# Optimization experiments

Measured on AMD Instinct MI355X. Metric: run time of the kernel, lower is better.

## Reference

```python
import jax, jax.numpy as jnp
import numpy as np

EPS = 1e-5

def _proj_bn(x, w, b, gamma, beta, mean, var):
    # 1x1 conv: [B,C,H,W] x [O,C] -> [B,O,H,W], then inference BatchNorm
    y = jnp.einsum('bchw,oc->bohw', x, w) + b[None, :, None, None]
    inv = gamma / jnp.sqrt(var + EPS)
    return y * inv[None, :, None, None] + (beta - mean * inv)[None, :, None, None]


def setup_inputs() -> dict:
    key = jax.random.key(0)
    ks = jax.random.split(key, 20)
    B, C, H, W = 4, 256, 64, 64
    Cq = C // 8
    s = lambda k, shp, sc: jax.random.normal(k, shp, dtype=jnp.float32) * sc
    inp = {
        'x1': s(ks[0], (B, C, H, W), 1.0),
        'x2': s(ks[1], (B, C, H, W), 1.0),
        'q_w': s(ks[2], (Cq, C), 0.05), 'q_b': s(ks[3], (Cq,), 0.02),
        'q_gamma': 1.0 + s(ks[4], (Cq,), 0.02), 'q_beta': s(ks[5], (Cq,), 0.02),
        'q_mean': s(ks[6], (Cq,), 0.1), 'q_var': jnp.abs(1.0 + s(ks[7], (Cq,), 0.1)),
        'k_w': s(ks[8], (Cq, C), 0.05), 'k_b': s(ks[9], (Cq,), 0.02),
        'k_gamma': 1.0 + s(ks[10], (Cq,), 0.02), 'k_beta': s(ks[11], (Cq,), 0.02),
        'k_mean': s(ks[12], (Cq,), 0.1), 'k_var': jnp.abs(1.0 + s(ks[13], (Cq,), 0.1)),
        'v_w': s(ks[14], (C, C), 0.05), 'v_b': s(ks[15], (C,), 0.02),
        'v_gamma': 1.0 + s(ks[16], (C,), 0.02), 'v_beta': s(ks[17], (C,), 0.02),
        'v_mean': s(ks[18], (C,), 0.1), 'v_var': jnp.abs(1.0 + s(ks[19], (C,), 0.1)),
    }
    return inp


def reference(x1, x2, q_w, q_b, q_gamma, q_beta, q_mean, q_var,
              k_w, k_b, k_gamma, k_beta, k_mean, k_var,
              v_w, v_b, v_gamma, v_beta, v_mean, v_var):
    B, C, H, W = x1.shape
    N = H * W
    dqk = C // 8
    q = _proj_bn(x1, q_w, q_b, q_gamma, q_beta, q_mean, q_var).reshape(B, dqk, N)  # [B,dqk,N]
    k = _proj_bn(x2, k_w, k_b, k_gamma, k_beta, k_mean, k_var).reshape(B, dqk, N)  # [B,dqk,N]
    v = _proj_bn(x2, v_w, v_b, v_gamma, v_beta, v_mean, v_var).reshape(B, C, N)    # [B,C,N]
    scale = 1.0 / np.sqrt(dqk).astype(np.float32)
    energy = jnp.einsum('bdm,bdn->bmn', q, k) * scale        # [B,N,N]
    attn = jax.nn.softmax(energy, axis=-1)
    out = jnp.einsum('bcn,bmn->bcm', v, attn)                # [B,C,N]
    return out.reshape(B, C, H, W)
```

## Files before the change

kernel.cpp:

```cpp
#include <hip/hip_runtime.h>

using short8   = __attribute__((ext_vector_type(8))) short;
using f32x4    = __attribute__((ext_vector_type(4))) float;
using ushort4v = __attribute__((ext_vector_type(4))) unsigned short;

#define BN_EPS 1e-5f
#define ATT_SCALE_LOG2E 0.2550348347988049f

__device__ __forceinline__ unsigned short f2bf(float f) {
    union { float f; unsigned u; } v; v.f = f;
    return (unsigned short)((v.u + 0x7FFFu + ((v.u >> 16) & 1u)) >> 16);
}

__device__ __forceinline__ unsigned pack2bf(float a, float b) {
    union { float f; unsigned u; } ua, ub; ua.f = a; ub.f = b;
    return __builtin_amdgcn_perm(ub.u + 0x8000u, ua.u + 0x8000u, 0x07060302u);
}

__device__ __forceinline__ void glds16(const void* gp, void* lp) {
    __builtin_amdgcn_global_load_lds(
        (const __attribute__((address_space(1))) unsigned*)gp,
        (__attribute__((address_space(3))) unsigned*)lp, 16, 0, 0);
}

__global__ void prep_kernel(
    const float* __restrict__ qw, const float* __restrict__ qb,
    const float* __restrict__ qg, const float* __restrict__ qbe,
    const float* __restrict__ qm, const float* __restrict__ qv,
    const float* __restrict__ kw, const float* __restrict__ kb,
    const float* __restrict__ kg, const float* __restrict__ kbe,
    const float* __restrict__ km, const float* __restrict__ kvv,
    const float* __restrict__ vw, const float* __restrict__ vb,
    const float* __restrict__ vg, const float* __restrict__ vbe,
    const float* __restrict__ vm, const float* __restrict__ vv,
    unsigned short* __restrict__ wq, float* __restrict__ scale,
    float* __restrict__ off)
{
    int r = blockIdx.x;
    int t = threadIdx.x;
    const float *wsrc, *g, *be, *mn, *vr, *bi;
    int rl;
    if (r < 32)      { rl = r;      wsrc = qw; g = qg; be = qbe; mn = qm; vr = qv;  bi = qb; }
    else if (r < 64) { rl = r - 32; wsrc = kw; g = kg; be = kbe; mn = km; vr = kvv; bi = kb; }
    else             { rl = r - 64; wsrc = vw; g = vg; be = vbe; mn = vm; vr = vv;  bi = vb; }

    float4 w4 = *(const float4*)(wsrc + rl * 256 + t * 4);
    ushort4v o;
    o.x = f2bf(w4.x); o.y = f2bf(w4.y); o.z = f2bf(w4.z); o.w = f2bf(w4.w);
    *(ushort4v*)(wq + r * 256 + t * 4) = o;

    if (t == 0) {
        float inv = g[rl] * rsqrtf(vr[rl] + BN_EPS);
        float ofv = bi[rl] * inv + be[rl] - mn[rl] * inv;
        float s = (r < 32) ? ATT_SCALE_LOG2E : 1.0f;
        scale[r] = inv * s;
        off[r]   = ofv * s;
    }
}

#define XT_PITCH 264

__global__ __launch_bounds__(256, 4) void proj_kernel(
    const float* __restrict__ x1, const float* __restrict__ x2,
    const unsigned short* __restrict__ wq,
    const float* __restrict__ scale, const float* __restrict__ off,
    unsigned short* __restrict__ q_t, unsigned short* __restrict__ k_t,
    unsigned short* __restrict__ v_ws)
{
    __shared__ __align__(16) unsigned short Xt[64 * XT_PITCH];
    int bx = blockIdx.x;
    int g  = bx >> 8;
    int t2 = bx & 255;
    int nt = t2 & 63;
    int b  = t2 >> 6;
    int n0 = nt * 64;
    int tid = threadIdx.x;
    int wv = tid >> 6, lane = tid & 63;
    int m16 = lane & 15, qd = lane >> 4;

    const float* xb = ((g == 0) ? x1 : x2) + (size_t)b * 256 * 4096 + n0 + lane;

    #pragma unroll 2
    for (int i = 0; i < 8; ++i) {
        int o = wv * 8 + i;
        const float* src = xb + (size_t)(o * 8) * 4096;
        uint4 dw;
        dw.x = pack2bf(src[0],                src[(size_t)1 * 4096]);
        dw.y = pack2bf(src[(size_t)2 * 4096], src[(size_t)3 * 4096]);
        dw.z = pack2bf(src[(size_t)4 * 4096], src[(size_t)5 * 4096]);
        dw.w = pack2bf(src[(size_t)6 * 4096], src[(size_t)7 * 4096]);
        *(uint4*)&Xt[lane * XT_PITCH + o * 8] = dw;
    }
    __syncthreads();

    f32x4 zero4 = {0.f, 0.f, 0.f, 0.f};

    if (g < 2) {
        int rb = g * 32;
        f32x4 acc0 = zero4, acc1 = zero4;
        #pragma unroll 2
        for (int s = 0; s < 8; ++s) {
            short8 w0 = *(const short8*)(wq + (size_t)(rb +      m16) * 256 + s * 32 + qd * 8);
            short8 w1 = *(const short8*)(wq + (size_t)(rb + 16 + m16) * 256 + s * 32 + qd * 8);
            short8 xf = *(const short8*)&Xt[(16 * wv + m16) * XT_PITCH + s * 32 + qd * 8];
            acc0 = __builtin_amdgcn_mfma_f32_16x16x32_bf16(w0, xf, acc0, 0, 0, 0);
            acc1 = __builtin_amdgcn_mfma_f32_16x16x32_bf16(w1, xf, acc1, 0, 0, 0);
        }
        unsigned short* dst = (g == 0) ? q_t : k_t;
        int ncol = n0 + 16 * wv + m16;
        #pragma unroll
        for (int tm = 0; tm < 2; ++tm) {
            f32x4 acc = tm ? acc1 : acc0;
            int r0 = 16 * tm + 4 * qd;
            float4 sc = *(const float4*)(scale + rb + r0);
            float4 of = *(const float4*)(off   + rb + r0);
            ushort4v o;
            o.x = f2bf(acc.x * sc.x + of.x);
            o.y = f2bf(acc.y * sc.y + of.y);
            o.z = f2bf(acc.z * sc.z + of.z);
            o.w = f2bf(acc.w * sc.w + of.w);
            *(ushort4v*)(dst + ((size_t)b * 4096 + ncol) * 32 + r0) = o;
        }
    } else {
        f32x4 acc[4][4];
        #pragma unroll
        for (int rr = 0; rr < 4; ++rr)
            #pragma unroll
            for (int tm = 0; tm < 4; ++tm) acc[rr][tm] = zero4;
        #pragma unroll 1
        for (int s = 0; s < 8; ++s) {
            short8 xf[4];
            #pragma unroll
            for (int tm = 0; tm < 4; ++tm)
                xf[tm] = *(const short8*)&Xt[(16 * tm + m16) * XT_PITCH + s * 32 + qd * 8];
            #pragma unroll
            for (int rr = 0; rr < 4; ++rr) {
                short8 wf = *(const short8*)(wq + (size_t)(64 + rr * 64 + 16 * wv + m16) * 256 + s * 32 + qd * 8);
                #pragma unroll
                for (int tm = 0; tm < 4; ++tm)
                    acc[rr][tm] = __builtin_amdgcn_mfma_f32_16x16x32_bf16(xf[tm], wf, acc[rr][tm], 0, 0, 0);
            }
        }
        unsigned short* vt = v_ws + ((size_t)b * 32 + (nt >> 1)) * 32768;
        int h = nt & 1;
        #pragma unroll
        for (int rr = 0; rr < 4; ++rr) {
            int c = rr * 64 + 16 * wv + m16;
            float sc = scale[64 + c], of = off[64 + c];
            #pragma unroll
            for (int tm = 0; tm < 4; ++tm) {
                int gg = 4 * tm + qd;
                int gs = (gg & 8) | ((gg & 7) ^ (c & 7));
                ushort4v o;
                o.x = f2bf(acc[rr][tm].x * sc + of);
                o.y = f2bf(acc[rr][tm].y * sc + of);
                o.z = f2bf(acc[rr][tm].z * sc + of);
                o.w = f2bf(acc[rr][tm].w * sc + of);
                *(ushort4v*)(vt + c * 128 + gs * 8 + h * 4) = o;
            }
        }
    }
}

__global__ __launch_bounds__(256, 2) void flash_kernel(
    const unsigned short* __restrict__ q_t, const unsigned short* __restrict__ k_t,
    const unsigned short* __restrict__ v_ws, float* __restrict__ out)
{
    __shared__ __align__(16) unsigned char Vb[2][32768];
    __shared__ __align__(16) float Lsh[256];

    int bx = blockIdx.x;
    int cg = (bx >> 2) & 1;
    int b  = bx & 3;
    int qg = bx >> 3;
    int q0 = qg * 64;
    int cb = cg * 128;

    int tid = threadIdx.x;
    int wv  = tid >> 6, lane = tid & 63;
    int m16 = lane & 15, qd = lane >> 4;

    const char* vpb = (const char*)v_ws + (size_t)b * 2097152 + (size_t)cb * 256;
    int vgo[8], vl[8];
    #pragma unroll
    for (int u = 0; u < 8; ++u) {
        int i = (wv * 8 + u) * 64 + lane;
        vgo[u] = i * 16;
        vl[u]  = (wv * 8 + u) * 1024;
    }
    int gw = wv * 4 + qd;
    int gs = (gw & 8) | ((gw & 7) ^ (m16 & 7));
    int vro[8];
    #pragma unroll
    for (int ct = 0; ct < 8; ++ct) vro[ct] = (ct * 16 + m16) * 256 + gs * 16;

    const unsigned short* kbase = k_t + ((size_t)b * 4096 + wv * 16 + m16) * 32 + qd * 8;

    const unsigned short* qb = q_t + ((size_t)b * 4096 + q0) * 32;
    short8 Qf[4];
    #pragma unroll
    for (int qt = 0; qt < 4; ++qt)
        Qf[qt] = *(const short8*)(qb + (size_t)(qt * 16 + m16) * 32 + qd * 8);

    f32x4 zero4 = {0.f, 0.f, 0.f, 0.f};
    f32x4 acc[4][8];
    #pragma unroll
    for (int qt = 0; qt < 4; ++qt)
        #pragma unroll
        for (int ct = 0; ct < 8; ++ct) acc[qt][ct] = zero4;
    float lsum[4] = {0.f, 0.f, 0.f, 0.f};

    #pragma unroll
    for (int u = 0; u < 8; ++u) glds16(vpb + vgo[u], (char*)Vb + vl[u]);
    short8 KA0 = *(const short8*)kbase;
    short8 KA1 = *(const short8*)(kbase + 2048);
    short8 KB0 = KA0, KB1 = KA1;

    auto body = [&](const short8& K0c, const short8& K1c,
                    short8& K0n, short8& K1n,
                    char* Vcur, char* Vnxt, int ep) {
        asm volatile("s_waitcnt vmcnt(0)\n\ts_barrier" ::: "memory");

        if (ep < 31) {
            const char* vs = vpb + (size_t)(ep + 1) * 65536;
            #pragma unroll
            for (int u = 0; u < 8; ++u) glds16(vs + vgo[u], Vnxt + vl[u]);
            const unsigned short* ks = kbase + (size_t)(ep + 1) * 4096;
            K0n = *(const short8*)ks;
            K1n = *(const short8*)(ks + 2048);
        }

        f32x4 SA[4], SB[4];
        #pragma unroll
        for (int qt = 0; qt < 4; ++qt) {
            SA[qt] = __builtin_amdgcn_mfma_f32_16x16x32_bf16(K0c, Qf[qt], zero4, 0, 0, 0);
            SB[qt] = __builtin_amdgcn_mfma_f32_16x16x32_bf16(K1c, Qf[qt], zero4, 0, 0, 0);
        }

        short8 ap[4];
        #pragma unroll
        for (int qt = 0; qt < 4; ++qt) {
            float a0 = __builtin_amdgcn_exp2f(SA[qt].x), a1 = __builtin_amdgcn_exp2f(SA[qt].y);
            float a2 = __builtin_amdgcn_exp2f(SA[qt].z), a3 = __builtin_amdgcn_exp2f(SA[qt].w);
            float b0 = __builtin_amdgcn_exp2f(SB[qt].x), b1 = __builtin_amdgcn_exp2f(SB[qt].y);
            float b2 = __builtin_amdgcn_exp2f(SB[qt].z), b3 = __builtin_amdgcn_exp2f(SB[qt].w);
            lsum[qt] += ((a0 + a1) + (a2 + a3)) + ((b0 + b1) + (b2 + b3));
            union { uint4 u; short8 s; } w;
            w.u.x = pack2bf(a0, a1); w.u.y = pack2bf(a2, a3);
            w.u.z = pack2bf(b0, b1); w.u.w = pack2bf(b2, b3);
            ap[qt] = w.s;
        }

        __builtin_amdgcn_s_setprio(1);
        #pragma unroll
        for (int ct = 0; ct < 8; ++ct) {
            short8 Vf = *(const short8*)(Vcur + vro[ct]);
            #pragma unroll
            for (int qt = 0; qt < 4; ++qt)
                acc[qt][ct] = __builtin_amdgcn_mfma_f32_16x16x32_bf16(ap[qt], Vf, acc[qt][ct], 0, 0, 0);
        }
        __builtin_amdgcn_s_setprio(0);
    };

    #pragma unroll 1
    for (int ep = 0; ep < 32; ep += 2) {
        body(KA0, KA1, KB0, KB1, (char*)Vb[0], (char*)Vb[1], ep);
        body(KB0, KB1, KA0, KA1, (char*)Vb[1], (char*)Vb[0], ep + 1);
    }

    #pragma unroll
    for (int qt = 0; qt < 4; ++qt) {
        float l = lsum[qt];
        l += __shfl_xor(l, 16);
        l += __shfl_xor(l, 32);
        if (lane < 16) Lsh[wv * 64 + qt * 16 + lane] = l;
    }

    char* X = (char*)Vb;
    asm volatile("s_waitcnt vmcnt(0) lgkmcnt(0)\n\ts_barrier" ::: "memory");
    if (wv >= 2) {
        char* dst = X + (size_t)(wv - 2) * 32768;
        #pragma unroll
        for (int qt = 0; qt < 4; ++qt)
            #pragma unroll
            for (int ct = 0; ct < 8; ++ct)
                *(f32x4*)(dst + (qt * 8 + ct) * 1024 + lane * 16) = acc[qt][ct];
    }
    asm volatile("s_waitcnt lgkmcnt(0)\n\ts_barrier" ::: "memory");
    if (wv < 2) {
        const char* src = X + (size_t)wv * 32768;
        #pragma unroll
        for (int qt = 0; qt < 4; ++qt)
            #pragma unroll
            for (int ct = 0; ct < 8; ++ct)
                acc[qt][ct] += *(const f32x4*)(src + (qt * 8 + ct) * 1024 + lane * 16);
    }
    asm volatile("s_waitcnt lgkmcnt(0)\n\ts_barrier" ::: "memory");
    if (wv == 1) {
        char* dst = X + 32768;
        #pragma unroll
        for (int qt = 0; qt < 4; ++qt)
            #pragma unroll
            for (int ct = 0; ct < 8; ++ct)
                *(f32x4*)(dst + (qt * 8 + ct) * 1024 + lane * 16) = acc[qt][ct];
    }
    asm volatile("s_waitcnt lgkmcnt(0)\n\ts_barrier" ::: "memory");
    if (wv == 0) {
        const char* src = X + 32768;
        #pragma unroll
        for (int qt = 0; qt < 4; ++qt)
            #pragma unroll
            for (int ct = 0; ct < 8; ++ct)
                acc[qt][ct] += *(const f32x4*)(src + (qt * 8 + ct) * 1024 + lane * 16);

        #pragma unroll
        for (int qt = 0; qt < 4; ++qt) {
            f32x4 s4 = *(const f32x4*)&Lsh[qt * 16 + qd * 4];
            s4 += *(const f32x4*)&Lsh[64  + qt * 16 + qd * 4];
            s4 += *(const f32x4*)&Lsh[128 + qt * 16 + qd * 4];
            s4 += *(const f32x4*)&Lsh[192 + qt * 16 + qd * 4];
            f32x4 inv4;
            inv4.x = __builtin_amdgcn_rcpf(s4.x);
            inv4.y = __builtin_amdgcn_rcpf(s4.y);
            inv4.z = __builtin_amdgcn_rcpf(s4.z);
            inv4.w = __builtin_amdgcn_rcpf(s4.w);
            #pragma unroll
            for (int ct = 0; ct < 8; ++ct) {
                float* ob = out + ((size_t)(b * 256 + cb + ct * 16 + m16)) * 4096
                                + q0 + qt * 16 + qd * 4;
                float4 o;
                o.x = acc[qt][ct].x * inv4.x;
                o.y = acc[qt][ct].y * inv4.y;
                o.z = acc[qt][ct].z * inv4.z;
                o.w = acc[qt][ct].w * inv4.w;
                *(float4*)ob = o;
            }
        }
    }
}

extern "C" void kernel_launch(void* const* d_in, const int* in_sizes, int n_in,
                              void* d_out, int out_size, void* d_ws, size_t ws_size,
                              hipStream_t stream)
{
    const float* x1  = (const float*)d_in[0];
    const float* x2  = (const float*)d_in[1];
    const float* qw  = (const float*)d_in[2];
    const float* qb  = (const float*)d_in[3];
    const float* qg  = (const float*)d_in[4];
    const float* qbe = (const float*)d_in[5];
    const float* qm  = (const float*)d_in[6];
    const float* qv  = (const float*)d_in[7];
    const float* kw  = (const float*)d_in[8];
    const float* kb  = (const float*)d_in[9];
    const float* kg  = (const float*)d_in[10];
    const float* kbe = (const float*)d_in[11];
    const float* km  = (const float*)d_in[12];
    const float* kvv = (const float*)d_in[13];
    const float* vw  = (const float*)d_in[14];
    const float* vb  = (const float*)d_in[15];
    const float* vg  = (const float*)d_in[16];
    const float* vbe = (const float*)d_in[17];
    const float* vm  = (const float*)d_in[18];
    const float* vv  = (const float*)d_in[19];

    char* ws = (char*)d_ws;
    unsigned short* wq   = (unsigned short*)(ws + 0);
    float*          scale= (float*)(ws + 163840);
    float*          off  = (float*)(ws + 165120);
    unsigned short* q_t  = (unsigned short*)(ws + 166400);
    unsigned short* k_t  = (unsigned short*)(ws + 166400 + 1048576);
    unsigned short* v_ws = (unsigned short*)(ws + 166400 + 2097152);

    prep_kernel<<<320, 64, 0, stream>>>(qw, qb, qg, qbe, qm, qv,
                                        kw, kb, kg, kbe, km, kvv,
                                        vw, vb, vg, vbe, vm, vv,
                                        wq, scale, off);
    proj_kernel<<<768, 256, 0, stream>>>(x1, x2, wq, scale, off, q_t, k_t, v_ws);
    flash_kernel<<<512, 256, 0, stream>>>(q_t, k_t, v_ws, (float*)d_out);
}
```

Before: 173.2 us.

## Software-pipeline attention loop: compute next tile's QK/exp during current PV

Restructures the main attention loop so the QK^T MFMA and exp2 for tile ep+1 are computed in the same iteration as the PV MFMAs for tile ep, with a prologue and epilogue. K and V loads are prefetched two tiles ahead, using partial vmcnt waits. All V fragments are read from LDS up front, and a second barrier guards reuse of the V buffer. This aims to hide exp/softmax latency and global-load latency behind matrix work, at the cost of more registers (two P fragment sets, eight V fragments) and an extra barrier per step.

```diff
diff --git a/kernel.cpp b/kernel.cpp
--- a/kernel.cpp
+++ b/kernel.cpp
@@ -210,62 +210,111 @@
         for (int ct = 0; ct < 8; ++ct) acc[qt][ct] = zero4;
     float lsum[4] = {0.f, 0.f, 0.f, 0.f};
 
-    #pragma unroll
-    for (int u = 0; u < 8; ++u) glds16(vpb + vgo[u], (char*)Vb + vl[u]);
     short8 KA0 = *(const short8*)kbase;
     short8 KA1 = *(const short8*)(kbase + 2048);
-    short8 KB0 = KA0, KB1 = KA1;
-
-    auto body = [&](const short8& K0c, const short8& K1c,
-                    short8& K0n, short8& K1n,
-                    char* Vcur, char* Vnxt, int ep) {
-        asm volatile("s_waitcnt vmcnt(0)\n\ts_barrier" ::: "memory");
-
-        if (ep < 31) {
-            const char* vs = vpb + (size_t)(ep + 1) * 65536;
-            #pragma unroll
-            for (int u = 0; u < 8; ++u) glds16(vs + vgo[u], Vnxt + vl[u]);
-            const unsigned short* ks = kbase + (size_t)(ep + 1) * 4096;
-            K0n = *(const short8*)ks;
-            K1n = *(const short8*)(ks + 2048);
-        }
+    short8 KB0 = *(const short8*)(kbase + 4096);
+    short8 KB1 = *(const short8*)(kbase + 4096 + 2048);
+    #pragma unroll
+    for (int u = 0; u < 8; ++u) glds16(vpb + vgo[u], (char*)Vb + vl[u]);
+    #pragma unroll
+    for (int u = 0; u < 8; ++u) glds16(vpb + 65536 + vgo[u], (char*)Vb[1] + vl[u]);
+    asm volatile("s_waitcnt vmcnt(16)" ::: "memory");
+
+    short8 apA[4], apB[4];
+    #pragma unroll
+    for (int qt = 0; qt < 4; ++qt) {
+        f32x4 SA = __builtin_amdgcn_mfma_f32_16x16x32_bf16(KA0, Qf[qt], zero4, 0, 0, 0);
+        f32x4 SB = __builtin_amdgcn_mfma_f32_16x16x32_bf16(KA1, Qf[qt], zero4, 0, 0, 0);
+        float a0 = __builtin_amdgcn_exp2f(SA.x), a1 = __builtin_amdgcn_exp2f(SA.y);
+        float a2 = __builtin_amdgcn_exp2f(SA.z), a3 = __builtin_amdgcn_exp2f(SA.w);
+        float b0 = __builtin_amdgcn_exp2f(SB.x), b1 = __builtin_amdgcn_exp2f(SB.y);
+        float b2 = __builtin_amdgcn_exp2f(SB.z), b3 = __builtin_amdgcn_exp2f(SB.w);
+        lsum[qt] += ((a0 + a1) + (a2 + a3)) + ((b0 + b1) + (b2 + b3));
+        union { uint4 u; short8 s; } w;
+        w.u.x = pack2bf(a0, a1); w.u.y = pack2bf(a2, a3);
+        w.u.z = pack2bf(b0, b1); w.u.w = pack2bf(b2, b3);
+        apA[qt] = w.s;
+    }
+
+    auto body = [&](short8 (&apC)[4], short8 (&apN)[4],
+                    const short8& Ku0, const short8& Ku1,
+                    short8& Kl0, short8& Kl1, int ep) {
+        asm volatile("s_waitcnt vmcnt(8)\n\ts_barrier" ::: "memory");
+        char* Vcur = (char*)Vb + (size_t)(ep & 1) * 32768;
+
+        short8 Vf[8];
+        #pragma unroll
+        for (int ct = 0; ct < 8; ++ct)
+            Vf[ct] = *(const short8*)(Vcur + vro[ct]);
 
         f32x4 SA[4], SB[4];
-        #pragma unroll
-        for (int qt = 0; qt < 4; ++qt) {
-            SA[qt] = __builtin_amdgcn_mfma_f32_16x16x32_bf16(K0c, Qf[qt], zero4, 0, 0, 0);
-            SB[qt] = __builtin_amdgcn_mfma_f32_16x16x32_bf16(K1c, Qf[qt], zero4, 0, 0, 0);
-        }
-
-        short8 ap[4];
-        #pragma unroll
-        for (int qt = 0; qt < 4; ++qt) {
-            float a0 = __builtin_amdgcn_exp2f(SA[qt].x), a1 = __builtin_amdgcn_exp2f(SA[qt].y);
-            float a2 = __builtin_amdgcn_exp2f(SA[qt].z), a3 = __builtin_amdgcn_exp2f(SA[qt].w);
-            float b0 = __builtin_amdgcn_exp2f(SB[qt].x), b1 = __builtin_amdgcn_exp2f(SB[qt].y);
-            float b2 = __builtin_amdgcn_exp2f(SB[qt].z), b3 = __builtin_amdgcn_exp2f(SB[qt].w);
-            lsum[qt] += ((a0 + a1) + (a2 + a3)) + ((b0 + b1) + (b2 + b3));
-            union { uint4 u; short8 s; } w;
-            w.u.x = pack2bf(a0, a1); w.u.y = pack2bf(a2, a3);
-            w.u.z = pack2bf(b0, b1); w.u.w = pack2bf(b2, b3);
-            ap[qt] = w.s;
+        bool doQK = (ep < 31);
+        if (doQK) {
+            #pragma unroll
+            for (int qt = 0; qt < 4; ++qt) {
+                SA[qt] = __builtin_amdgcn_mfma_f32_16x16x32_bf16(Ku0, Qf[qt], zero4, 0, 0, 0);
+                SB[qt] = __builtin_amdgcn_mfma_f32_16x16x32_bf16(Ku1, Qf[qt], zero4, 0, 0, 0);
+            }
+        }
+
+        asm volatile("s_waitcnt lgkmcnt(0)\n\ts_barrier" ::: "memory");
+
+        if (ep < 30) {
+            const unsigned short* ks = kbase + (size_t)(ep + 2) * 4096;
+            Kl0 = *(const short8*)ks;
+            Kl1 = *(const short8*)(ks + 2048);
+            const char* vs = vpb + (size_t)(ep + 2) * 65536;
+            #pragma unroll
+            for (int u = 0; u < 8; ++u) glds16(vs + vgo[u], Vcur + vl[u]);
+        }
+
+        if (doQK) {
+            #pragma unroll
+            for (int qt = 0; qt < 4; ++qt) {
+                float a0 = __builtin_amdgcn_exp2f(SA[qt].x), a1 = __builtin_amdgcn_exp2f(SA[qt].y);
+                float a2 = __builtin_amdgcn_exp2f(SA[qt].z), a3 = __builtin_amdgcn_exp2f(SA[qt].w);
+                float b0 = __builtin_amdgcn_exp2f(SB[qt].x), b1 = __builtin_amdgcn_exp2f(SB[qt].y);
+                float b2 = __builtin_amdgcn_exp2f(SB[qt].z), b3 = __builtin_amdgcn_exp2f(SB[qt].w);
+                lsum[qt] += ((a0 + a1) + (a2 + a3)) + ((b0 + b1) + (b2 + b3));
+                union { uint4 u; short8 s; } w;
+                w.u.x = pack2bf(a0, a1); w.u.y = pack2bf(a2, a3);
+                w.u.z = pack2bf(b0, b1); w.u.w = pack2bf(b2, b3);
+                apN[qt] = w.s;
+            }
         }
 
         __builtin_amdgcn_s_setprio(1);
         #pragma unroll
         for (int ct = 0; ct < 8; ++ct) {
-            short8 Vf = *(const short8*)(Vcur + vro[ct]);
             #pragma unroll
             for (int qt = 0; qt < 4; ++qt)
-                acc[qt][ct] = __builtin_amdgcn_mfma_f32_16x16x32_bf16(ap[qt], Vf, acc[qt][ct], 0, 0, 0);
+                acc[qt][ct] = __builtin_amdgcn_mfma_f32_16x16x32_bf16(apC[qt], Vf[ct], acc[qt][ct], 0, 0, 0);
         }
         __builtin_amdgcn_s_setprio(0);
     };
 
     #pragma unroll 1
-    for (int ep = 0; ep < 32; ep += 2) {
-        body(KA0, KA1, KB0, KB1, (char*)Vb[0], (char*)Vb[1], ep);
-        body(KB0, KB1, KA0, KA1, (char*)Vb[1], (char*)Vb[0], ep + 1);
+    for (int ep = 0; ep < 30; ep += 2) {
+        body(apA, apB, KB0, KB1, KA0, KA1, ep);
+        body(apB, apA, KA0, KA1, KB0, KB1, ep + 1);
+    }
+    body(apA, apB, KB0, KB1, KA0, KA1, 30);
+
+    {
+        asm volatile("s_waitcnt vmcnt(0)\n\ts_barrier" ::: "memory");
+        char* Vcur = (char*)Vb + 32768;
+        short8 Vf[8];
+        #pragma unroll
+        for (int ct = 0; ct < 8; ++ct)
+            Vf[ct] = *(const short8*)(Vcur + vro[ct]);
+        __builtin_amdgcn_s_setprio(1);
+        #pragma unroll
+        for (int ct = 0; ct < 8; ++ct) {
+            #pragma unroll
+            for (int qt = 0; qt < 4; ++qt)
+                acc[qt][ct] = __builtin_amdgcn_mfma_f32_16x16x32_bf16(apB[qt], Vf[ct], acc[qt][ct], 0, 0, 0);
+        }
+        __builtin_amdgcn_s_setprio(0);
     }
 
     #pragma unroll
```

New measurement: 423.9 us. 145% more time.
